# Performance work log

Hardware: AMD Instinct MI355X
Metric: run time of the kernel (lower is better)

Reference implementation:

```python
import jax, jax.numpy as jnp
import numpy as np

M, N, DIM = 32, 32, 128
BATCH = 2048
NITER = 100
ALPHA = 0.3
SIGMA = max(M, N) / 2.0


def setup_inputs() -> dict:
    key = jax.random.key(0)
    k1, k2 = jax.random.split(key)
    x = jax.random.normal(k1, (BATCH, DIM), dtype=jnp.float32)
    weights = jax.random.normal(k2, (M * N, DIM), dtype=jnp.float32)
    # Grid locations exactly as in the torch module (meshgrid, ravel, transpose)
    xx, yy = np.meshgrid(np.linspace(0, M - 1, M), np.linspace(0, N - 1, N))
    locations = jnp.asarray(
        np.array((xx.ravel(), yy.ravel())).T.astype(np.int32)
    )  # [mn, 2]
    return {"x": x, "weights": weights, "locations": locations, "it": 5}


def reference(x, weights, locations, it):
    # --- BMU search: pairwise Euclidean distances weights [mn,d] vs x [b,d] ---
    # argmin over squared distances == argmin over cdist (sqrt is monotone)
    w2 = jnp.sum(weights * weights, axis=1)  # [mn]
    x2 = jnp.sum(x * x, axis=1)              # [b]
    d2 = w2[:, None] + x2[None, :] - 2.0 * (weights @ x.T)  # [mn, b]
    bmu_idx = jnp.argmin(d2, axis=0)         # [b]
    bmu_locs = locations[bmu_idx]            # [b, 2]

    # --- linearly decayed learning rate / neighbourhood width ---
    lr_decay = 1.0 - it / NITER
    alpha_op = ALPHA * lr_decay
    sigma_op = SIGMA * lr_decay

    # --- gaussian neighbourhood over grid distances: [mn, b] ---
    locf = locations.astype(jnp.float32)
    bmuf = bmu_locs.astype(jnp.float32)
    bmu_d2 = jnp.sum((locf[:, None, :] - bmuf[None, :, :]) ** 2, axis=2)  # [mn, b]
    lr_op = alpha_op * jnp.exp(-bmu_d2 / (sigma_op * sigma_op))           # [mn, b]

    # --- delta = sum_b lr_op[:, b] * (x[b] - w)  (algebraically reduced) ---
    # == lr_op @ x - rowsum(lr_op) * weights; avoids the [mn, b, d] intermediate
    delta = lr_op @ x - jnp.sum(lr_op, axis=1, keepdims=True) * weights  # [mn, d]
    return weights + delta
```

## Files before the change

kernel.cpp:

```cpp
#include <hip/hip_runtime.h>
#include <stdint.h>

#define DIM   128
#define MN    1024
#define BATCH 2048
#define ALPHA 0.3f
#define SIGMA 16.0f
#define LOG2E 1.44269504088896f


__global__ __launch_bounds__(256) void init_kernel(
    unsigned long long* __restrict__ keys, float4* __restrict__ Sq)
{
  const int t = threadIdx.x;
  if (blockIdx.x < 8) {
    keys[blockIdx.x * 256 + t] = ~0ull;
  } else {
    int i = (blockIdx.x - 8) * 256 + t;
    if (i < (524288 + 4096) / 16)
      Sq[i] = make_float4(0.f, 0.f, 0.f, 0.f);
  }
}

__global__ __launch_bounds__(256) void bmu_kernel(
    const float* __restrict__ x, const float* __restrict__ w,
    unsigned long long* __restrict__ keys)
{
  __shared__ __align__(16) float wt[64][36];
  __shared__ __align__(16) float xt[128][36];
  __shared__ unsigned long long bkey[128];

  const int t  = threadIdx.x;
  const int tu = t & 15;
  const int tb = t >> 4;
  const int u0 = (blockIdx.x & 15) * 64;
  const int b0 = (blockIdx.x >> 4) * 128;

  if (t < 128) bkey[t] = ~0ull;

  float acc[4][8];
  float w2[4];
#pragma unroll
  for (int i = 0; i < 4; ++i) {
    w2[i] = 0.f;
#pragma unroll
    for (int j = 0; j < 8; ++j) acc[i][j] = 0.f;
  }

  for (int kt = 0; kt < 4; ++kt) {
    const int k0 = kt * 32;
    __syncthreads();
#pragma unroll
    for (int r = 0; r < 2; ++r) {
      int idx = t + 256 * r;
      int uu = idx >> 3, kq = idx & 7;
      float4 v = *reinterpret_cast<const float4*>(&w[(u0 + uu) * DIM + k0 + kq * 4]);
      *reinterpret_cast<float4*>(&wt[uu][kq * 4]) = v;
    }
#pragma unroll
    for (int r = 0; r < 4; ++r) {
      int idx = t + 256 * r;
      int bb = idx >> 3, kq = idx & 7;
      float4 v = *reinterpret_cast<const float4*>(&x[(b0 + bb) * DIM + k0 + kq * 4]);
      *reinterpret_cast<float4*>(&xt[bb][kq * 4]) = v;
    }
    __syncthreads();
#pragma unroll
    for (int kq = 0; kq < 8; ++kq) {
      float4 aq[4];
#pragma unroll
      for (int i = 0; i < 4; ++i)
        aq[i] = *reinterpret_cast<const float4*>(&wt[tu + 16 * i][kq * 4]);
#pragma unroll
      for (int i = 0; i < 4; ++i)
        w2[i] += aq[i].x * aq[i].x + aq[i].y * aq[i].y +
                 aq[i].z * aq[i].z + aq[i].w * aq[i].w;
#pragma unroll
      for (int j = 0; j < 8; ++j) {
        float4 bq = *reinterpret_cast<const float4*>(&xt[tb + 16 * j][kq * 4]);
#pragma unroll
        for (int i = 0; i < 4; ++i) {
          acc[i][j] += aq[i].x * bq.x + aq[i].y * bq.y +
                       aq[i].z * bq.z + aq[i].w * bq.w;
        }
      }
    }
  }

#pragma unroll
  for (int j = 0; j < 8; ++j) {
    unsigned long long kmin = ~0ull;
#pragma unroll
    for (int i = 0; i < 4; ++i) {
      float s = w2[i] - 2.0f * acc[i][j];
      unsigned int sb = __float_as_uint(s);
      sb ^= (sb >> 31) ? 0xFFFFFFFFu : 0x80000000u;
      unsigned long long key =
          ((unsigned long long)sb << 32) | (unsigned int)(u0 + tu + 16 * i);
      if (key < kmin) kmin = key;
    }
    atomicMin(&bkey[tb + 16 * j], kmin);
  }
  __syncthreads();
  if (tu == 0) {
#pragma unroll
    for (int j = 0; j < 8; ++j) {
      int lb = tb + 16 * j;
      atomicMin(&keys[b0 + lb], bkey[lb]);
    }
  }
}

__global__ __launch_bounds__(256) void scatter_kernel(
    const float* __restrict__ x, const unsigned long long* __restrict__ keys,
    float* __restrict__ S, float* __restrict__ cnt)
{
  int idx = blockIdx.x * 256 + threadIdx.x;
  if (idx >= BATCH * 33) return;
  int b  = (int)((unsigned int)idx / 33u);
  int cq = idx - b * 33;
  unsigned int v = (unsigned int)keys[b];
  if (cq < 32) {
    float4 xv = *reinterpret_cast<const float4*>(&x[b * DIM + cq * 4]);
    float* Sv = S + v * DIM + cq * 4;
    unsafeAtomicAdd(&Sv[0], xv.x);
    unsafeAtomicAdd(&Sv[1], xv.y);
    unsafeAtomicAdd(&Sv[2], xv.z);
    unsafeAtomicAdd(&Sv[3], xv.w);
  } else {
    unsafeAtomicAdd(&cnt[v], 1.0f);
  }
}

__global__ __launch_bounds__(256) void convfinal_kernel(
    const float* __restrict__ S, const float* __restrict__ cnt,
    const float* __restrict__ w, const int* __restrict__ itp,
    float* __restrict__ out)
{
  __shared__ float gxt[64], gyt[64];
  __shared__ __align__(16) float T4[1024][4];
  __shared__ float Tc[1024];

  const int t = threadIdx.x;
  const int q = blockIdx.x;

  const float lr_decay = 1.0f - (float)itp[0] * 0.01f;
  const float alpha_op = ALPHA * lr_decay;
  const float sg       = SIGMA * lr_decay;
  const float c2       = -LOG2E / (sg * sg);

  if (t < 63) {
    float dd = (float)(t - 31);
    float g = __builtin_amdgcn_exp2f(c2 * dd * dd);
    gxt[t] = g;
    gyt[t] = alpha_op * g;
  }
  __syncthreads();

#pragma unroll
  for (int r = 0; r < 4; ++r) {
    int p  = t + 256 * r;
    int vy = p >> 5, ux = p & 31;
    float a0 = 0.f, a1 = 0.f, a2 = 0.f, a3 = 0.f, ac = 0.f;
    const float* Srow = S + (vy * 32) * DIM + q * 4;
    const float* Crow = cnt + vy * 32;
#pragma unroll 4
    for (int vx = 0; vx < 32; ++vx) {
      float g = gxt[ux - vx + 31];
      float4 s4 = *reinterpret_cast<const float4*>(&Srow[vx * DIM]);
      a0 = fmaf(g, s4.x, a0); a1 = fmaf(g, s4.y, a1);
      a2 = fmaf(g, s4.z, a2); a3 = fmaf(g, s4.w, a3);
      ac = fmaf(g, Crow[vx], ac);
    }
    T4[p][0] = a0; T4[p][1] = a1; T4[p][2] = a2; T4[p][3] = a3;
    Tc[p] = ac;
  }
  __syncthreads();

#pragma unroll
  for (int r = 0; r < 4; ++r) {
    int p  = t + 256 * r;
    int uy = p >> 5, ux = p & 31;
    float d0 = 0.f, d1 = 0.f, d2 = 0.f, d3 = 0.f, rs = 0.f;
#pragma unroll 4
    for (int vy = 0; vy < 32; ++vy) {
      float g = gyt[uy - vy + 31];
      float4 t4 = *reinterpret_cast<const float4*>(&T4[vy * 32 + ux][0]);
      d0 = fmaf(g, t4.x, d0); d1 = fmaf(g, t4.y, d1);
      d2 = fmaf(g, t4.z, d2); d3 = fmaf(g, t4.w, d3);
      rs = fmaf(g, Tc[vy * 32 + ux], rs);
    }
    float4 wv = *reinterpret_cast<const float4*>(&w[p * DIM + q * 4]);
    float om = 1.0f - rs;
    float4 o;
    o.x = wv.x * om + d0;
    o.y = wv.y * om + d1;
    o.z = wv.z * om + d2;
    o.w = wv.w * om + d3;
    *reinterpret_cast<float4*>(&out[p * DIM + q * 4]) = o;
  }
}

extern "C" void kernel_launch(void* const* d_in, const int* in_sizes, int n_in,
                              void* d_out, int out_size, void* d_ws, size_t ws_size,
                              hipStream_t stream) {
  const float* x   = (const float*)d_in[0];
  const float* w   = (const float*)d_in[1];
  const int*   itp = (const int*)d_in[3];
  float* out = (float*)d_out;

  unsigned long long* keys = (unsigned long long*)d_ws;
  float* S   = (float*)((char*)d_ws + 16384);
  float* cnt = (float*)((char*)d_ws + 16384 + 524288);

  init_kernel<<<8 + 129, 256, 0, stream>>>(keys, (float4*)S);
  bmu_kernel<<<256, 256, 0, stream>>>(x, w, keys);
  scatter_kernel<<<(BATCH * 33 + 255) / 256, 256, 0, stream>>>(x, keys, S, cnt);
  convfinal_kernel<<<32, 256, 0, stream>>>(S, cnt, w, itp, out);
}
```

Measured before the change: 107.0 us.

## Compute BMU distances with split-fp16 MFMA instead of fp32 FMA

Rewrites the BMU distance GEMM to use 16x16x32 fp16 MFMA instructions. Each operand is split into high and low fp16 halves, and three products are summed to approximate fp32 accuracy. A prep kernel, merged with workspace zeroing, converts x and w to these halves and precomputes the squared weight norms. Each wave then loads its fragments straight from global memory and reduces argmin keys with shuffles. The aim is to remove the costly scalar fp32 FMA loop, at the cost of an extra conversion pass, more global traffic, and a small risk of argmin ties flipping from the reduced precision.

```diff
diff --git a/kernel.cpp b/kernel.cpp
--- a/kernel.cpp
+++ b/kernel.cpp
@@ -8,106 +8,119 @@
 #define SIGMA 16.0f
 #define LOG2E 1.44269504088896f
 
-
-__global__ __launch_bounds__(256) void init_kernel(
-    unsigned long long* __restrict__ keys, float4* __restrict__ Sq)
+typedef _Float16 half8 __attribute__((ext_vector_type(8)));
+typedef _Float16 half4 __attribute__((ext_vector_type(4)));
+typedef float    floatx4 __attribute__((ext_vector_type(4)));
+
+
+__global__ __launch_bounds__(256) void prep_kernel(
+    const float* __restrict__ x, const float* __restrict__ w,
+    unsigned long long* __restrict__ keys, float4* __restrict__ Sq,
+    float* __restrict__ w2,
+    _Float16* __restrict__ wh, _Float16* __restrict__ wl,
+    _Float16* __restrict__ xh, _Float16* __restrict__ xl)
 {
   const int t = threadIdx.x;
-  if (blockIdx.x < 8) {
-    keys[blockIdx.x * 256 + t] = ~0ull;
+  const int bid = blockIdx.x;
+  if (bid < 8) {
+    keys[bid * 256 + t] = ~0ull;
+  } else if (bid < 137) {
+    int i = (bid - 8) * 256 + t;
+    Sq[i] = make_float4(0.f, 0.f, 0.f, 0.f);
+  } else if (bid < 145) {
+    int idx = (bid - 137) * 256 + t;
+    int row = idx >> 1, half = idx & 1;
+    int base = row * DIM + half * 64;
+    float s = 0.f;
+#pragma unroll
+    for (int q = 0; q < 16; ++q) {
+      float4 v = *reinterpret_cast<const float4*>(&w[base + q * 4]);
+      s += v.x * v.x + v.y * v.y + v.z * v.z + v.w * v.w;
+      half4 h, l;
+      h[0] = (_Float16)v.x; l[0] = (_Float16)(v.x - (float)h[0]);
+      h[1] = (_Float16)v.y; l[1] = (_Float16)(v.y - (float)h[1]);
+      h[2] = (_Float16)v.z; l[2] = (_Float16)(v.z - (float)h[2]);
+      h[3] = (_Float16)v.w; l[3] = (_Float16)(v.w - (float)h[3]);
+      *reinterpret_cast<half4*>(&wh[base + q * 4]) = h;
+      *reinterpret_cast<half4*>(&wl[base + q * 4]) = l;
+    }
+    s += __shfl_xor(s, 1);
+    if (!half) w2[row] = s;
   } else {
-    int i = (blockIdx.x - 8) * 256 + t;
-    if (i < (524288 + 4096) / 16)
-      Sq[i] = make_float4(0.f, 0.f, 0.f, 0.f);
-  }
-}
-
-__global__ __launch_bounds__(256) void bmu_kernel(
-    const float* __restrict__ x, const float* __restrict__ w,
-    unsigned long long* __restrict__ keys)
-{
-  __shared__ __align__(16) float wt[64][36];
-  __shared__ __align__(16) float xt[128][36];
-  __shared__ unsigned long long bkey[128];
-
-  const int t  = threadIdx.x;
-  const int tu = t & 15;
-  const int tb = t >> 4;
-  const int u0 = (blockIdx.x & 15) * 64;
-  const int b0 = (blockIdx.x >> 4) * 128;
-
-  if (t < 128) bkey[t] = ~0ull;
-
-  float acc[4][8];
-  float w2[4];
-#pragma unroll
-  for (int i = 0; i < 4; ++i) {
-    w2[i] = 0.f;
-#pragma unroll
-    for (int j = 0; j < 8; ++j) acc[i][j] = 0.f;
-  }
-
-  for (int kt = 0; kt < 4; ++kt) {
-    const int k0 = kt * 32;
-    __syncthreads();
-#pragma unroll
-    for (int r = 0; r < 2; ++r) {
-      int idx = t + 256 * r;
-      int uu = idx >> 3, kq = idx & 7;
-      float4 v = *reinterpret_cast<const float4*>(&w[(u0 + uu) * DIM + k0 + kq * 4]);
-      *reinterpret_cast<float4*>(&wt[uu][kq * 4]) = v;
-    }
-#pragma unroll
-    for (int r = 0; r < 4; ++r) {
-      int idx = t + 256 * r;
-      int bb = idx >> 3, kq = idx & 7;
-      float4 v = *reinterpret_cast<const float4*>(&x[(b0 + bb) * DIM + k0 + kq * 4]);
-      *reinterpret_cast<float4*>(&xt[bb][kq * 4]) = v;
-    }
-    __syncthreads();
-#pragma unroll
-    for (int kq = 0; kq < 8; ++kq) {
-      float4 aq[4];
-#pragma unroll
-      for (int i = 0; i < 4; ++i)
-        aq[i] = *reinterpret_cast<const float4*>(&wt[tu + 16 * i][kq * 4]);
-#pragma unroll
-      for (int i = 0; i < 4; ++i)
-        w2[i] += aq[i].x * aq[i].x + aq[i].y * aq[i].y +
-                 aq[i].z * aq[i].z + aq[i].w * aq[i].w;
-#pragma unroll
-      for (int j = 0; j < 8; ++j) {
-        float4 bq = *reinterpret_cast<const float4*>(&xt[tb + 16 * j][kq * 4]);
-#pragma unroll
-        for (int i = 0; i < 4; ++i) {
-          acc[i][j] += aq[i].x * bq.x + aq[i].y * bq.y +
-                       aq[i].z * bq.z + aq[i].w * bq.w;
-        }
-      }
-    }
-  }
-
-#pragma unroll
-  for (int j = 0; j < 8; ++j) {
+    int idx = (bid - 145) * 256 + t;
+    int row = idx >> 2, part = idx & 3;
+    int base = row * DIM + part * 32;
+#pragma unroll
+    for (int q = 0; q < 8; ++q) {
+      float4 v = *reinterpret_cast<const float4*>(&x[base + q * 4]);
+      half4 h, l;
+      h[0] = (_Float16)v.x; l[0] = (_Float16)(v.x - (float)h[0]);
+      h[1] = (_Float16)v.y; l[1] = (_Float16)(v.y - (float)h[1]);
+      h[2] = (_Float16)v.z; l[2] = (_Float16)(v.z - (float)h[2]);
+      h[3] = (_Float16)v.w; l[3] = (_Float16)(v.w - (float)h[3]);
+      *reinterpret_cast<half4*>(&xh[base + q * 4]) = h;
+      *reinterpret_cast<half4*>(&xl[base + q * 4]) = l;
+    }
+  }
+}
+
+__global__ __launch_bounds__(64) void bmu_kernel(
+    const _Float16* __restrict__ xh, const _Float16* __restrict__ xl,
+    const _Float16* __restrict__ wh, const _Float16* __restrict__ wl,
+    const float* __restrict__ w2, unsigned long long* __restrict__ keys)
+{
+  const int lane = threadIdx.x;
+  const int u0 = (blockIdx.x & 63) * 16;
+  const int b0 = (blockIdx.x >> 6) * 128;
+  const int r  = lane & 15;
+  const int q  = lane >> 4;
+
+  half8 Ah[4], Al[4];
+  {
+    const _Float16* wrh = wh + (u0 + r) * DIM + q * 8;
+    const _Float16* wrl = wl + (u0 + r) * DIM + q * 8;
+#pragma unroll
+    for (int c = 0; c < 4; ++c) {
+      Ah[c] = *reinterpret_cast<const half8*>(wrh + c * 32);
+      Al[c] = *reinterpret_cast<const half8*>(wrl + c * 32);
+    }
+  }
+  float w2r[4];
+#pragma unroll
+  for (int i = 0; i < 4; ++i) w2r[i] = w2[u0 + q * 4 + i];
+
+#pragma unroll
+  for (int bt = 0; bt < 8; ++bt) {
+    const int b = b0 + bt * 16;
+    const _Float16* xrh = xh + (b + r) * DIM + q * 8;
+    const _Float16* xrl = xl + (b + r) * DIM + q * 8;
+    half8 Bh[4], Bl[4];
+#pragma unroll
+    for (int c = 0; c < 4; ++c) {
+      Bh[c] = *reinterpret_cast<const half8*>(xrh + c * 32);
+      Bl[c] = *reinterpret_cast<const half8*>(xrl + c * 32);
+    }
+    floatx4 acc = {0.f, 0.f, 0.f, 0.f};
+#pragma unroll
+    for (int c = 0; c < 4; ++c) {
+      acc = __builtin_amdgcn_mfma_f32_16x16x32_f16(Ah[c], Bh[c], acc, 0, 0, 0);
+      acc = __builtin_amdgcn_mfma_f32_16x16x32_f16(Ah[c], Bl[c], acc, 0, 0, 0);
+      acc = __builtin_amdgcn_mfma_f32_16x16x32_f16(Al[c], Bh[c], acc, 0, 0, 0);
+    }
     unsigned long long kmin = ~0ull;
 #pragma unroll
     for (int i = 0; i < 4; ++i) {
-      float s = w2[i] - 2.0f * acc[i][j];
+      float s = w2r[i] - 2.0f * acc[i];
       unsigned int sb = __float_as_uint(s);
       sb ^= (sb >> 31) ? 0xFFFFFFFFu : 0x80000000u;
       unsigned long long key =
-          ((unsigned long long)sb << 32) | (unsigned int)(u0 + tu + 16 * i);
+          ((unsigned long long)sb << 32) | (unsigned int)(u0 + q * 4 + i);
       if (key < kmin) kmin = key;
     }
-    atomicMin(&bkey[tb + 16 * j], kmin);
-  }
-  __syncthreads();
-  if (tu == 0) {
-#pragma unroll
-    for (int j = 0; j < 8; ++j) {
-      int lb = tb + 16 * j;
-      atomicMin(&keys[b0 + lb], bkey[lb]);
-    }
+    unsigned long long o;
+    o = __shfl_xor(kmin, 16); if (o < kmin) kmin = o;
+    o = __shfl_xor(kmin, 32); if (o < kmin) kmin = o;
+    if (lane < 16) atomicMin(&keys[b + r], kmin);
   }
 }
 
@@ -209,12 +222,18 @@
   const int*   itp = (const int*)d_in[3];
   float* out = (float*)d_out;
 
-  unsigned long long* keys = (unsigned long long*)d_ws;
-  float* S   = (float*)((char*)d_ws + 16384);
-  float* cnt = (float*)((char*)d_ws + 16384 + 524288);
-
-  init_kernel<<<8 + 129, 256, 0, stream>>>(keys, (float4*)S);
-  bmu_kernel<<<256, 256, 0, stream>>>(x, w, keys);
+  char* ws = (char*)d_ws;
+  unsigned long long* keys = (unsigned long long*)ws;
+  float*     S   = (float*)(ws + 16384);
+  float*     cnt = (float*)(ws + 540672);
+  float*     w2  = (float*)(ws + 544768);
+  _Float16*  wh  = (_Float16*)(ws + 548864);
+  _Float16*  wl  = (_Float16*)(ws + 811008);
+  _Float16*  xh  = (_Float16*)(ws + 1073152);
+  _Float16*  xl  = (_Float16*)(ws + 1597440);
+
+  prep_kernel<<<177, 256, 0, stream>>>(x, w, keys, (float4*)S, w2, wh, wl, xh, xl);
+  bmu_kernel<<<1024, 64, 0, stream>>>(xh, xl, wh, wl, w2, keys);
   scatter_kernel<<<(BATCH * 33 + 255) / 256, 256, 0, stream>>>(x, keys, S, cnt);
   convfinal_kernel<<<32, 256, 0, stream>>>(S, cnt, w, itp, out);
 }
```

After: 107.2 us. Within noise of the previous version (+0.2%).
